# Performance work log

Measured on AMD Instinct MI355X. Metric: run time of the kernel, lower is better.

The kernel has to match this reference:

```python
import jax, jax.numpy as jnp
import numpy as np

# Mamba2 derived dims (headdim=64, ngroups=1, mamba_ssm defaults)
D_MODEL = 1024
D_STATE = 64
D_CONV = 4
EXPAND = 2
D_INNER = EXPAND * D_MODEL          # 2048
HEADDIM = 64
NHEADS = D_INNER // HEADDIM          # 32
CONV_DIM = D_INNER + 2 * D_STATE     # 2176 (x, B, C share the depthwise conv)
D_IN_PROJ = 2 * D_INNER + 2 * D_STATE + NHEADS  # 4256 (z, xBC, dt)
BATCH, SEQ = 8, 1024


def setup_inputs() -> dict:
    key = jax.random.key(0)
    ks = jax.random.split(key, 8)
    g = lambda k, shp, sc=0.02: (jax.random.normal(k, shp, jnp.float32) * sc)
    # dt_bias init as in mamba_ssm: inverse-softplus of dt ~ U[1e-3, 1e-1] (log-uniform)
    dt = jnp.exp(jax.random.uniform(ks[3], (NHEADS,), jnp.float32)
                 * (jnp.log(0.1) - jnp.log(0.001)) + jnp.log(0.001))
    dt_bias = dt + jnp.log(-jnp.expm1(-dt))  # softplus^{-1}(dt)
    A_log = jnp.log(jax.random.uniform(ks[4], (NHEADS,), jnp.float32, 1.0, 16.0))
    return {
        "x": jax.random.normal(ks[0], (BATCH, SEQ, D_MODEL), jnp.float32),
        "W_in": g(ks[1], (D_MODEL, D_IN_PROJ)),
        "conv_w": g(ks[2], (D_CONV, CONV_DIM), 0.2),
        "conv_b": jnp.zeros((CONV_DIM,), jnp.float32),
        "dt_bias": dt_bias,
        "A_log": A_log,
        "Dskip": jnp.ones((NHEADS,), jnp.float32),
        "norm_w": jnp.ones((D_INNER,), jnp.float32),
        "W_out": g(ks[5], (D_INNER, D_MODEL)),
        "head_w": g(ks[6], (D_MODEL, 1)),
        "head_b": jnp.zeros((1,), jnp.float32),
    }


def _mamba2(x, W_in, conv_w, conv_b, dt_bias, A_log, Dskip, norm_w, W_out):
    b, l, _ = x.shape
    zxbcdt = x @ W_in                                   # (b, l, 4256)
    z = zxbcdt[..., :D_INNER]
    xBC = zxbcdt[..., D_INNER:D_INNER + CONV_DIM]
    dt = jax.nn.softplus(zxbcdt[..., D_INNER + CONV_DIM:] + dt_bias)  # (b, l, h)
    # causal depthwise conv1d (kernel D_CONV) + SiLU
    pad = jnp.pad(xBC, ((0, 0), (D_CONV - 1, 0), (0, 0)))
    conv = conv_b + sum(pad[:, k:k + l, :] * conv_w[k] for k in range(D_CONV))
    xBC = jax.nn.silu(conv)
    xh = xBC[..., :D_INNER].reshape(b, l, NHEADS, HEADDIM)
    B = xBC[..., D_INNER:D_INNER + D_STATE]             # (b, l, s) ngroups=1
    C = xBC[..., D_INNER + D_STATE:]                    # (b, l, s)
    A = -jnp.exp(A_log)                                 # (h,)
    dA = jnp.exp(dt * A)                                # (b, l, h)

    def step(h, inps):
        dA_t, dt_t, B_t, C_t, x_t = inps                # (b,h),(b,h),(b,s),(b,s),(b,h,p)
        h = h * dA_t[:, :, None, None] + (dt_t[:, :, None] * x_t)[..., None] * B_t[:, None, None, :]
        y = jnp.einsum('bhps,bs->bhp', h, C_t)
        return h, y

    tm = lambda a: jnp.moveaxis(a, 1, 0)                # time-major for scan
    h0 = jnp.zeros((b, NHEADS, HEADDIM, D_STATE), x.dtype)
    _, y = jax.lax.scan(step, h0, (tm(dA), tm(dt), tm(B), tm(C), tm(xh)))
    y = jnp.moveaxis(y, 0, 1) + Dskip[None, None, :, None] * xh   # skip connection
    # gated RMSNorm: norm(y * silu(z)) * weight
    y = y.reshape(b, l, D_INNER) * jax.nn.silu(z)
    y = y * jax.lax.rsqrt(jnp.mean(y * y, axis=-1, keepdims=True) + 1e-5) * norm_w
    return y @ W_out                                    # (b, l, d_model)


def reference(x, W_in, conv_w, conv_b, dt_bias, A_log, Dskip, norm_w, W_out, head_w, head_b):
    y = _mamba2(x, W_in, conv_w, conv_b, dt_bias, A_log, Dskip, norm_w, W_out)
    return y @ head_w + head_b                          # (b, l, 1)
```

## Files before the change

### kernel.cpp

```cpp
#include <hip/hip_runtime.h>
#include <hip/hip_bf16.h>

#define D_MODEL   1024
#define D_STATE   64
#define D_INNER   2048
#define NHEADS    32
#define CONV_DIM  2176
#define D_IN_PROJ 4256
#define NPAD      4352
#define BATCH     8
#define SEQ       1024
#define NROWS     8192
#define NCHUNK    8
#define CLEN      128

typedef __attribute__((ext_vector_type(8))) short bf16x8;
typedef __attribute__((ext_vector_type(4))) float f32x4;

__device__ __forceinline__ float bf2f(unsigned short u){
  unsigned v = ((unsigned)u) << 16;
  return __builtin_bit_cast(float, v);
}
__device__ __forceinline__ unsigned short f2bf(float f){
  __hip_bfloat16 h = __float2bfloat16(f);
  return __builtin_bit_cast(unsigned short, h);
}

__global__ __launch_bounds__(256) void k_convert_x(const float* __restrict__ x,
                                                   unsigned short* __restrict__ xb){
  int i = blockIdx.x*256 + threadIdx.x;
  float4 v = ((const float4*)x)[i];
  ushort4 o;
  o.x = f2bf(v.x); o.y = f2bf(v.y); o.z = f2bf(v.z); o.w = f2bf(v.w);
  ((ushort4*)xb)[i] = o;
}

__global__ __launch_bounds__(256) void k_transpose_win(const float* __restrict__ W_in,
                                                       unsigned short* __restrict__ wt){
  __shared__ float tile[32][33];
  int n0 = blockIdx.x * 32;
  int k0 = blockIdx.y * 32;
  int tx = threadIdx.x & 31;
  int ty = threadIdx.x >> 5;
  #pragma unroll
  for (int i = 0; i < 4; ++i){
    int kk = ty + i*8;
    int n  = n0 + tx;
    tile[kk][tx] = (n < D_IN_PROJ) ? W_in[(size_t)(k0+kk)*D_IN_PROJ + n] : 0.f;
  }
  __syncthreads();
  #pragma unroll
  for (int i = 0; i < 4; ++i){
    int nn = ty + i*8;
    wt[(size_t)(n0+nn)*D_MODEL + k0 + tx] = f2bf(tile[tx][nn]);
  }
}

__global__ __launch_bounds__(256) void k_nwc(const float* __restrict__ W_out,
                                             const float* __restrict__ head_w,
                                             const float* __restrict__ norm_w,
                                             float* __restrict__ nwc){
  int d    = blockIdx.x*4 + (threadIdx.x >> 6);
  int lane = threadIdx.x & 63;
  const float* row = W_out + (size_t)d * D_MODEL;
  float s = 0.f;
  #pragma unroll
  for (int k = lane; k < D_MODEL; k += 64) s += row[k] * head_w[k];
  #pragma unroll
  for (int off = 32; off; off >>= 1) s += __shfl_down(s, off);
  if (lane == 0) nwc[d] = s * norm_w[d];
}

__global__ __launch_bounds__(256) void k_gemm_bf16_bt(const unsigned short* __restrict__ A,
                                                      const unsigned short* __restrict__ BT,
                                                      unsigned short* __restrict__ C,
                                                      int M, int N, int K){
  __shared__ unsigned short aT[128*64];
  __shared__ unsigned short bT[128*64];
  int nb   = N >> 7;
  int bid  = blockIdx.x;
  int swz  = (bid & 7) * (gridDim.x >> 3) + (bid >> 3);
  int m0   = (swz / nb) << 7;
  int n0   = (swz % nb) << 7;
  int tid  = threadIdx.x;
  int wid  = tid >> 6, lane = tid & 63;
  int wr   = wid >> 1, wc = wid & 1;

  f32x4 acc[4][4];
  #pragma unroll
  for (int i = 0; i < 4; ++i)
    #pragma unroll
    for (int j = 0; j < 4; ++j)
      acc[i][j] = (f32x4){0.f, 0.f, 0.f, 0.f};

  int frow = lane & 15;
  int fk   = (lane >> 4) << 3;
  int srow = lane >> 3;
  int skk  = (lane & 7) << 3;

  for (int k0 = 0; k0 < K; k0 += 64){
    __syncthreads();
    #pragma unroll
    for (int it = 0; it < 4; ++it){
      int ch  = (wid << 2) | it;
      int row = (ch << 3) | srow;
      __builtin_amdgcn_global_load_lds(
        (const __attribute__((address_space(1))) void*)(A  + (size_t)(m0+row)*K + k0 + skk),
        (__attribute__((address_space(3))) void*)(aT + (ch << 9)), 16, 0, 0);
      __builtin_amdgcn_global_load_lds(
        (const __attribute__((address_space(1))) void*)(BT + (size_t)(n0+row)*K + k0 + skk),
        (__attribute__((address_space(3))) void*)(bT + (ch << 9)), 16, 0, 0);
    }
    __syncthreads();
    #pragma unroll
    for (int kk = 0; kk < 64; kk += 32){
      bf16x8 af[4], bfv[4];
      #pragma unroll
      for (int i = 0; i < 4; ++i)
        af[i]  = *(const bf16x8*)(aT + ((wr*64 + i*16 + frow) << 6) + kk + fk);
      #pragma unroll
      for (int j = 0; j < 4; ++j)
        bfv[j] = *(const bf16x8*)(bT + ((wc*64 + j*16 + frow) << 6) + kk + fk);
      #pragma unroll
      for (int i = 0; i < 4; ++i)
        #pragma unroll
        for (int j = 0; j < 4; ++j)
          acc[i][j] = __builtin_amdgcn_mfma_f32_16x16x32_bf16(af[i], bfv[j], acc[i][j], 0, 0, 0);
    }
  }

  int crow = (lane >> 4) << 2;
  int ccol = lane & 15;
  #pragma unroll
  for (int i = 0; i < 4; ++i)
    #pragma unroll
    for (int j = 0; j < 4; ++j){
      size_t base = (size_t)(m0 + wr*64 + i*16 + crow) * N + (n0 + wc*64 + j*16 + ccol);
      #pragma unroll
      for (int r = 0; r < 4; ++r)
        C[base + (size_t)r * N] = f2bf(acc[i][j][r]);
    }
}

__global__ __launch_bounds__(256) void k_dtda(const unsigned short* __restrict__ zx,
                                              const float* __restrict__ dt_bias,
                                              float* __restrict__ dtb){
  int i = blockIdx.x*256 + threadIdx.x;
  int r = i >> 5, h = i & 31;
  float raw = bf2f(zx[(size_t)r*NPAD + D_INNER + CONV_DIM + h]) + dt_bias[h];
  float dt  = (raw > 20.f) ? raw : log1pf(expf(raw));
  int b = r >> 10, l = r & 1023;
  dtb[(b*32 + h)*1024 + l] = dt;
}

__global__ __launch_bounds__(256) void k_conv(const unsigned short* __restrict__ zx,
                                              const float* __restrict__ conv_w,
                                              const float* __restrict__ conv_b,
                                              unsigned short* __restrict__ xbc,
                                              unsigned short* __restrict__ bc16){
  int r = blockIdx.x;
  int l = r & (SEQ - 1);
  for (int oc = threadIdx.x; oc < 272; oc += 256){
    int c = oc * 8;
    float acc[8];
    #pragma unroll
    for (int j = 0; j < 8; ++j) acc[j] = conv_b[c + j];
    #pragma unroll
    for (int k = 0; k < 4; ++k){
      int dl = l + k - 3;
      if (dl >= 0){
        bf16x8 v = *(const bf16x8*)(zx + (size_t)(r + k - 3)*NPAD + D_INNER + c);
        #pragma unroll
        for (int j = 0; j < 8; ++j)
          acc[j] = fmaf(bf2f((unsigned short)v[j]), conv_w[k*CONV_DIM + c + j], acc[j]);
      }
    }
    bf16x8 o;
    #pragma unroll
    for (int j = 0; j < 8; ++j){
      float s = acc[j] / (1.f + expf(-acc[j]));
      o[j] = (short)f2bf(s);
    }
    if (c < D_INNER) *(bf16x8*)(xbc  + (size_t)r*D_INNER + c) = o;
    else             *(bf16x8*)(bc16 + (size_t)r*128 + (c - D_INNER)) = o;
  }
}

__global__ __launch_bounds__(64) void k_cs(const float* __restrict__ dtb,
                                           const float* __restrict__ A_log,
                                           float* __restrict__ csb,
                                           float* __restrict__ cumA){
  int id = blockIdx.x;
  int bh = id >> 3, c = id & 7;
  int h  = bh & 31;
  int l  = threadIdx.x;
  const float* src = dtb + (size_t)bh*1024 + (c << 7);
  float d0 = src[2*l], d1 = src[2*l + 1];
  float pr = d0 + d1;
  float s  = pr;
  #pragma unroll
  for (int off = 1; off < 64; off <<= 1){
    float n = __shfl_up(s, off);
    if (l >= off) s += n;
  }
  float excl = s - pr;
  csb[(size_t)id*128 + 2*l]     = excl + d0;
  csb[(size_t)id*128 + 2*l + 1] = excl + pr;
  if (l == 63){
    float A = -expf(A_log[h]);
    cumA[id] = expf(A * s);
  }
}

__global__ __launch_bounds__(256) void k_ssd1(const unsigned short* __restrict__ xbc,
                                              const unsigned short* __restrict__ bc16,
                                              const float* __restrict__ dtb,
                                              const float* __restrict__ csb,
                                              const float* __restrict__ A_log,
                                              unsigned short* __restrict__ hend){
  __shared__ __align__(16) unsigned short XTw[64*136];
  __shared__ __align__(16) unsigned short BTl[64*136];
  int id = blockIdx.x;
  int bh = id >> 3, c = id & 7;
  int b  = bh >> 5, h = bh & 31;
  int tid = threadIdx.x;
  int w = tid >> 6, l = tid & 63;
  float A = -expf(A_log[h]);
  int row0 = b*SEQ + (c << 7);
  float csT = csb[(size_t)id*128 + 127];

  #pragma unroll
  for (int it = 0; it < 4; ++it){
    int idx = it*256 + tid;
    int tau = idx >> 3, pb = idx & 7;
    bf16x8 v = *(const bf16x8*)(xbc + (size_t)(row0+tau)*D_INNER + h*64 + pb*8);
    float wgt = dtb[(size_t)bh*1024 + (c<<7) + tau]
              * expf(A*(csT - csb[(size_t)id*128 + tau]));
    #pragma unroll
    for (int j = 0; j < 8; ++j)
      XTw[(pb*8+j)*136 + tau] = f2bf(bf2f((unsigned short)v[j]) * wgt);
  }
  #pragma unroll
  for (int it = 0; it < 4; ++it){
    int idx = it*256 + tid;
    int tau = idx >> 3, sb = idx & 7;
    bf16x8 v = *(const bf16x8*)(bc16 + (size_t)(row0+tau)*128 + sb*8);
    #pragma unroll
    for (int j = 0; j < 8; ++j)
      BTl[(sb*8+j)*136 + tau] = (unsigned short)v[j];
  }
  __syncthreads();

  int fr = l & 15, fo = (l >> 4) << 3;
  f32x4 acc[4];
  #pragma unroll
  for (int n = 0; n < 4; ++n) acc[n] = (f32x4){0.f,0.f,0.f,0.f};
  #pragma unroll
  for (int kt = 0; kt < 4; ++kt){
    bf16x8 pf = *(const bf16x8*)(XTw + (w*16+fr)*136 + kt*32 + fo);
    #pragma unroll
    for (int n = 0; n < 4; ++n){
      bf16x8 qf = *(const bf16x8*)(BTl + (n*16+fr)*136 + kt*32 + fo);
      acc[n] = __builtin_amdgcn_mfma_f32_16x16x32_bf16(pf, qf, acc[n], 0, 0, 0);
    }
  }
  #pragma unroll
  for (int n = 0; n < 4; ++n)
    #pragma unroll
    for (int r = 0; r < 4; ++r){
      int p = w*16 + ((l>>4)<<2) + r;
      int s = n*16 + fr;
      hend[(size_t)id*4096 + p*64 + s] = f2bf(acc[n][r]);
    }
}

__global__ __launch_bounds__(256) void k_comb(unsigned short* __restrict__ hh,
                                              const float* __restrict__ cumA){
  int bh = blockIdx.x, tid = threadIdx.x;
  float carry[16];
  #pragma unroll
  for (int i = 0; i < 16; ++i) carry[i] = 0.f;
  #pragma unroll
  for (int c = 0; c < NCHUNK; ++c){
    size_t base = (((size_t)bh*NCHUNK + c) << 12) + tid*16;
    bf16x8 a0 = *(const bf16x8*)(hh + base);
    bf16x8 a1 = *(const bf16x8*)(hh + base + 8);
    float ca = cumA[bh*NCHUNK + c];
    float tmp[16];
    #pragma unroll
    for (int i = 0; i < 8; ++i){
      tmp[i]   = bf2f((unsigned short)a0[i]);
      tmp[8+i] = bf2f((unsigned short)a1[i]);
    }
    bf16x8 w0, w1;
    #pragma unroll
    for (int i = 0; i < 8; ++i){
      w0[i] = (short)f2bf(carry[i]);
      w1[i] = (short)f2bf(carry[8+i]);
    }
    *(bf16x8*)(hh + base)     = w0;
    *(bf16x8*)(hh + base + 8) = w1;
    #pragma unroll
    for (int i = 0; i < 16; ++i) carry[i] = tmp[i] + ca*carry[i];
  }
}

__global__ __launch_bounds__(256) void k_ssd2(const unsigned short* __restrict__ xbc,
                                              const unsigned short* __restrict__ bc16,
                                              const float* __restrict__ dtb,
                                              const float* __restrict__ csb,
                                              const float* __restrict__ A_log,
                                              const float* __restrict__ Dskip,
                                              const unsigned short* __restrict__ hbuf,
                                              unsigned short* __restrict__ yb){
  __shared__ __align__(16) unsigned short Bl[128*72];
  __shared__ __align__(16) unsigned short Cl[128*72];
  __shared__ __align__(16) unsigned short XTl[64*136];
  __shared__ __align__(16) unsigned short hl[64*72];
  __shared__ __align__(16) unsigned short Gm[128*136];
  __shared__ float cs_l[128], dt_l[128], a_l[128];

  int id = blockIdx.x;
  int bh = id >> 3, c = id & 7;
  int b  = bh >> 5, h = bh & 31;
  int tid = threadIdx.x;
  int w = tid >> 6, l = tid & 63;
  float A = -expf(A_log[h]);
  int row0 = b*SEQ + (c << 7);

  #pragma unroll
  for (int it = 0; it < 8; ++it){
    int idx = it*256 + tid;
    int tau = idx >> 4, cb = idx & 15;
    bf16x8 v = *(const bf16x8*)(bc16 + (size_t)(row0+tau)*128 + cb*8);
    unsigned short* dst = (cb < 8) ? (Bl + tau*72 + cb*8)
                                   : (Cl + tau*72 + (cb-8)*8);
    *(bf16x8*)dst = v;
  }
  #pragma unroll
  for (int it = 0; it < 4; ++it){
    int idx = it*256 + tid;
    int tau = idx >> 3, pb = idx & 7;
    bf16x8 v = *(const bf16x8*)(xbc + (size_t)(row0+tau)*D_INNER + h*64 + pb*8);
    #pragma unroll
    for (int j = 0; j < 8; ++j)
      XTl[(pb*8+j)*136 + tau] = (unsigned short)v[j];
  }
  #pragma unroll
  for (int it = 0; it < 2; ++it){
    int idx = it*256 + tid;
    int p = idx >> 3, sb = idx & 7;
    bf16x8 v = *(const bf16x8*)(hbuf + (size_t)id*4096 + p*64 + sb*8);
    *(bf16x8*)(hl + p*72 + sb*8) = v;
  }
  if (tid < 128){
    float cs = csb[(size_t)id*128 + tid];
    cs_l[tid] = cs;
    dt_l[tid] = dtb[(size_t)bh*1024 + (c<<7) + tid];
    a_l[tid]  = expf(A*cs);
  }
  __syncthreads();

  int fr = l & 15, fo = (l >> 4) << 3;
  int mtB = 7 - w;

  f32x4 Y[2][4];
  #pragma unroll
  for (int mi = 0; mi < 2; ++mi)
    #pragma unroll
    for (int n = 0; n < 4; ++n) Y[mi][n] = (f32x4){0.f,0.f,0.f,0.f};
  #pragma unroll
  for (int mi = 0; mi < 2; ++mi){
    int mt = mi ? mtB : w;
    #pragma unroll
    for (int kt = 0; kt < 2; ++kt){
      bf16x8 pf = *(const bf16x8*)(Cl + (mt*16+fr)*72 + kt*32 + fo);
      #pragma unroll
      for (int n = 0; n < 4; ++n){
        bf16x8 qf = *(const bf16x8*)(hl + (n*16+fr)*72 + kt*32 + fo);
        Y[mi][n] = __builtin_amdgcn_mfma_f32_16x16x32_bf16(pf, qf, Y[mi][n], 0, 0, 0);
      }
    }
    #pragma unroll
    for (int r = 0; r < 4; ++r){
      float av = a_l[mt*16 + ((l>>4)<<2) + r];
      #pragma unroll
      for (int n = 0; n < 4; ++n) Y[mi][n][r] *= av;
    }
  }

  f32x4 Sv[9];
  #pragma unroll
  for (int slot = 0; slot < 9; ++slot){
    int mt = (slot <= w) ? w : mtB;
    int nt = (slot <= w) ? slot : slot - w - 1;
    f32x4 acc = (f32x4){0.f,0.f,0.f,0.f};
    #pragma unroll
    for (int kt = 0; kt < 2; ++kt){
      bf16x8 pf = *(const bf16x8*)(Cl + (mt*16+fr)*72 + kt*32 + fo);
      bf16x8 qf = *(const bf16x8*)(Bl + (nt*16+fr)*72 + kt*32 + fo);
      acc = __builtin_amdgcn_mfma_f32_16x16x32_bf16(pf, qf, acc, 0, 0, 0);
    }
    int tau = nt*16 + fr;
    float dtt = dt_l[tau];
    float cst = cs_l[tau];
    #pragma unroll
    for (int r = 0; r < 4; ++r){
      int t = mt*16 + ((l>>4)<<2) + r;
      float v = acc[r] * dtt * expf(A*(cs_l[t] - cst));
      acc[r] = (tau <= t) ? v : 0.f;
    }
    Sv[slot] = acc;
  }

  __syncthreads();

  #pragma unroll
  for (int slot = 0; slot < 9; ++slot){
    int mt = (slot <= w) ? w : mtB;
    int nt = (slot <= w) ? slot : slot - w - 1;
    int tau = nt*16 + fr;
    #pragma unroll
    for (int r = 0; r < 4; ++r){
      int t = mt*16 + ((l>>4)<<2) + r;
      Gm[t*136 + tau] = f2bf(Sv[slot][r]);
    }
  }
  {
    int mtE = (w & 1) ? mtB : w;
    int ntE = mtE + 1;
    #pragma unroll
    for (int r = 0; r < 4; ++r){
      int t = mtE*16 + ((l>>4)<<2) + r;
      Gm[t*136 + ntE*16 + fr] = 0;
    }
  }
  __syncthreads();

  #pragma unroll
  for (int mi = 0; mi < 2; ++mi){
    int mt = mi ? mtB : w;
    int kmax = (mt + 2) >> 1;
    for (int kt2 = 0; kt2 < kmax; ++kt2){
      bf16x8 pf = *(const bf16x8*)(Gm + (mt*16+fr)*136 + kt2*32 + fo);
      #pragma unroll
      for (int n = 0; n < 4; ++n){
        bf16x8 qf = *(const bf16x8*)(XTl + (n*16+fr)*136 + kt2*32 + fo);
        Y[mi][n] = __builtin_amdgcn_mfma_f32_16x16x32_bf16(pf, qf, Y[mi][n], 0, 0, 0);
      }
    }
  }

  float dsk = Dskip[h];
  #pragma unroll
  for (int mi = 0; mi < 2; ++mi){
    int mt = mi ? mtB : w;
    #pragma unroll
    for (int r = 0; r < 4; ++r){
      int t = mt*16 + ((l>>4)<<2) + r;
      size_t orow = (size_t)(row0 + t)*D_INNER + h*64;
      #pragma unroll
      for (int n = 0; n < 4; ++n){
        int p = n*16 + fr;
        float xv = bf2f(XTl[p*136 + t]);
        yb[orow + p] = f2bf(Y[mi][n][r] + dsk*xv);
      }
    }
  }
}

__global__ __launch_bounds__(256) void k_epilogue(const unsigned short* __restrict__ y,
                                                  const unsigned short* __restrict__ zx,
                                                  const float* __restrict__ nwc,
                                                  const float* __restrict__ head_b,
                                                  float* __restrict__ out){
  int r   = blockIdx.x;
  int tid = threadIdx.x;
  bf16x8 y8 = *(const bf16x8*)(y  + (size_t)r*D_INNER + tid*8);
  bf16x8 z8 = *(const bf16x8*)(zx + (size_t)r*NPAD   + tid*8);
  float4 w0 = ((const float4*)nwc)[tid*2];
  float4 w1 = ((const float4*)nwc)[tid*2 + 1];
  float wv[8] = {w0.x, w0.y, w0.z, w0.w, w1.x, w1.y, w1.z, w1.w};
  float s2 = 0.f, sd = 0.f;
  #pragma unroll
  for (int k = 0; k < 8; ++k){
    float yf = bf2f((unsigned short)y8[k]);
    float zf = bf2f((unsigned short)z8[k]);
    float g  = yf * (zf / (1.f + expf(-zf)));
    s2 += g*g; sd += g*wv[k];
  }
  #pragma unroll
  for (int off = 32; off; off >>= 1){
    s2 += __shfl_down(s2, off);
    sd += __shfl_down(sd, off);
  }
  __shared__ float r2[4], rd[4];
  if ((tid & 63) == 0){ r2[tid >> 6] = s2; rd[tid >> 6] = sd; }
  __syncthreads();
  if (tid == 0){
    float t2 = r2[0] + r2[1] + r2[2] + r2[3];
    float td = rd[0] + rd[1] + rd[2] + rd[3];
    out[r] = rsqrtf(t2 * (1.f/2048.f) + 1e-5f) * td + head_b[0];
  }
}

extern "C" void kernel_launch(void* const* d_in, const int* in_sizes, int n_in,
                              void* d_out, int out_size, void* d_ws, size_t ws_size,
                              hipStream_t stream){
  const float* x       = (const float*)d_in[0];
  const float* W_in    = (const float*)d_in[1];
  const float* conv_w  = (const float*)d_in[2];
  const float* conv_b  = (const float*)d_in[3];
  const float* dt_bias = (const float*)d_in[4];
  const float* A_log   = (const float*)d_in[5];
  const float* Dskip   = (const float*)d_in[6];
  const float* norm_w  = (const float*)d_in[7];
  const float* W_out   = (const float*)d_in[8];
  const float* head_w  = (const float*)d_in[9];
  const float* head_b  = (const float*)d_in[10];
  float* out = (float*)d_out;

  char* ws = (char*)d_ws;
  unsigned short* xb   = (unsigned short*)(ws + 0);
  unsigned short* wt   = (unsigned short*)(ws + 16777216);
  unsigned short* zx16 = (unsigned short*)(ws + 25690112);
  unsigned short* xbc  = (unsigned short*)(ws + 96993280);
  float*          dtb  = (float*)         (ws + 132644864);
  float*          nwc  = (float*)         (ws + 134742016);
  unsigned short* yb   = (unsigned short*)(ws + 134750208);

  unsigned short* hbuf = xb;
  unsigned short* bc16 = wt;
  float*          csb  = (float*)(ws + 16777216 + 2097152);
  float*          cumA = (float*)(ws + 16777216 + 3145728);

  k_convert_x<<<8192, 256, 0, stream>>>(x, xb);
  k_transpose_win<<<dim3(136, 32), 256, 0, stream>>>(W_in, wt);
  k_nwc<<<512, 256, 0, stream>>>(W_out, head_w, norm_w, nwc);
  k_gemm_bf16_bt<<<(NROWS/128)*(NPAD/128), 256, 0, stream>>>(xb, wt, zx16, NROWS, NPAD, D_MODEL);
  k_dtda<<<1024, 256, 0, stream>>>(zx16, dt_bias, dtb);
  k_conv<<<NROWS, 256, 0, stream>>>(zx16, conv_w, conv_b, xbc, bc16);
  k_cs<<<2048, 64, 0, stream>>>(dtb, A_log, csb, cumA);
  k_ssd1<<<2048, 256, 0, stream>>>(xbc, bc16, dtb, csb, A_log, hbuf);
  k_comb<<<256, 256, 0, stream>>>(hbuf, cumA);
  k_ssd2<<<2048, 256, 0, stream>>>(xbc, bc16, dtb, csb, A_log, Dskip, hbuf, yb);
  k_epilogue<<<NROWS, 256, 0, stream>>>(yb, zx16, nwc, head_b, out);
}
```

Before: 280.4 us.

## Replace input-projection GEMM with 256x256 double-buffered tile kernel

Result: no change. 284.4 us (+1.4%).

```diff
diff --git a/kernel.cpp b/kernel.cpp
--- a/kernel.cpp
+++ b/kernel.cpp
@@ -71,74 +71,88 @@
   if (lane == 0) nwc[d] = s * norm_w[d];
 }
 
-__global__ __launch_bounds__(256) void k_gemm_bf16_bt(const unsigned short* __restrict__ A,
-                                                      const unsigned short* __restrict__ BT,
-                                                      unsigned short* __restrict__ C,
-                                                      int M, int N, int K){
-  __shared__ unsigned short aT[128*64];
-  __shared__ unsigned short bT[128*64];
-  int nb   = N >> 7;
+__global__ __launch_bounds__(512, 1) void k_gemm256(const unsigned short* __restrict__ A,
+                                                    const unsigned short* __restrict__ BT,
+                                                    unsigned short* __restrict__ C){
+  __shared__ unsigned short smem[65536];
   int bid  = blockIdx.x;
-  int swz  = (bid & 7) * (gridDim.x >> 3) + (bid >> 3);
-  int m0   = (swz / nb) << 7;
-  int n0   = (swz % nb) << 7;
+  int m0   = (bid / 17) << 8;
+  int n0   = (bid % 17) << 8;
   int tid  = threadIdx.x;
-  int wid  = tid >> 6, lane = tid & 63;
-  int wr   = wid >> 1, wc = wid & 1;
-
-  f32x4 acc[4][4];
-  #pragma unroll
-  for (int i = 0; i < 4; ++i)
-    #pragma unroll
-    for (int j = 0; j < 4; ++j)
-      acc[i][j] = (f32x4){0.f, 0.f, 0.f, 0.f};
-
-  int frow = lane & 15;
-  int fk   = (lane >> 4) << 3;
-  int srow = lane >> 3;
-  int skk  = (lane & 7) << 3;
-
-  for (int k0 = 0; k0 < K; k0 += 64){
-    __syncthreads();
-    #pragma unroll
-    for (int it = 0; it < 4; ++it){
-      int ch  = (wid << 2) | it;
-      int row = (ch << 3) | srow;
-      __builtin_amdgcn_global_load_lds(
-        (const __attribute__((address_space(1))) void*)(A  + (size_t)(m0+row)*K + k0 + skk),
-        (__attribute__((address_space(3))) void*)(aT + (ch << 9)), 16, 0, 0);
-      __builtin_amdgcn_global_load_lds(
-        (const __attribute__((address_space(1))) void*)(BT + (size_t)(n0+row)*K + k0 + skk),
-        (__attribute__((address_space(3))) void*)(bT + (ch << 9)), 16, 0, 0);
-    }
-    __syncthreads();
+  int w    = tid >> 6, lane = tid & 63;
+  int wr   = w >> 2, wc = w & 3;
+  int stR  = tid >> 3;
+  int stC  = (tid & 7) << 3;
+  int wb   = w << 9;
+
+  f32x4 acc[8][4];
+  #pragma unroll
+  for (int i = 0; i < 8; ++i)
+    #pragma unroll
+    for (int j = 0; j < 4; ++j) acc[i][j] = (f32x4){0.f,0.f,0.f,0.f};
+
+  const unsigned short* sA0 = A  + (size_t)(m0 + stR)*D_MODEL + stC;
+  const unsigned short* sB0 = BT + (size_t)(n0 + stR)*D_MODEL + stC;
+
+#define STAGE256(bb, kt) { \
+    const unsigned short* pa = sA0 + (size_t)(kt)*64; \
+    const unsigned short* pb = sB0 + (size_t)(kt)*64; \
+    _Pragma("unroll") \
+    for (int it = 0; it < 4; ++it){ \
+      __builtin_amdgcn_global_load_lds((const __attribute__((address_space(1))) void*)(pa + (size_t)it*64*D_MODEL), \
+          (__attribute__((address_space(3))) void*)(smem + (bb)*32768 + it*4096 + wb), 16, 0, 0); \
+      __builtin_amdgcn_global_load_lds((const __attribute__((address_space(1))) void*)(pb + (size_t)it*64*D_MODEL), \
+          (__attribute__((address_space(3))) void*)(smem + (bb)*32768 + 16384 + it*4096 + wb), 16, 0, 0); \
+    } }
+
+  STAGE256(0, 0);
+
+  int frow = lane & 15, fk = (lane >> 4) << 3;
+
+  for (int t = 0; t < 16; ++t){
+    int cur = t & 1;
+    asm volatile("" ::: "memory");
+    __builtin_amdgcn_s_barrier();
+    if (t < 15){
+      STAGE256(cur ^ 1, t + 1);
+      asm volatile("s_waitcnt vmcnt(8)" ::: "memory");
+    } else {
+      asm volatile("s_waitcnt vmcnt(0)" ::: "memory");
+    }
+    __builtin_amdgcn_s_barrier();
+    asm volatile("" ::: "memory");
+
+    const unsigned short* At = smem + cur*32768;
+    const unsigned short* Bt = At + 16384;
+    __builtin_amdgcn_s_setprio(1);
     #pragma unroll
     for (int kk = 0; kk < 64; kk += 32){
-      bf16x8 af[4], bfv[4];
-      #pragma unroll
-      for (int i = 0; i < 4; ++i)
-        af[i]  = *(const bf16x8*)(aT + ((wr*64 + i*16 + frow) << 6) + kk + fk);
-      #pragma unroll
-      for (int j = 0; j < 4; ++j)
-        bfv[j] = *(const bf16x8*)(bT + ((wc*64 + j*16 + frow) << 6) + kk + fk);
-      #pragma unroll
-      for (int i = 0; i < 4; ++i)
+      bf16x8 af[8], bfr[4];
+      #pragma unroll
+      for (int mf = 0; mf < 8; ++mf)
+        af[mf] = *(const bf16x8*)(At + (wr*128 + mf*16 + frow)*64 + kk + fk);
+      #pragma unroll
+      for (int nf = 0; nf < 4; ++nf)
+        bfr[nf] = *(const bf16x8*)(Bt + (wc*64 + nf*16 + frow)*64 + kk + fk);
+      #pragma unroll
+      for (int mf = 0; mf < 8; ++mf)
         #pragma unroll
-        for (int j = 0; j < 4; ++j)
-          acc[i][j] = __builtin_amdgcn_mfma_f32_16x16x32_bf16(af[i], bfv[j], acc[i][j], 0, 0, 0);
-    }
-  }
-
-  int crow = (lane >> 4) << 2;
-  int ccol = lane & 15;
-  #pragma unroll
-  for (int i = 0; i < 4; ++i)
-    #pragma unroll
-    for (int j = 0; j < 4; ++j){
-      size_t base = (size_t)(m0 + wr*64 + i*16 + crow) * N + (n0 + wc*64 + j*16 + ccol);
+        for (int nf = 0; nf < 4; ++nf)
+          acc[mf][nf] = __builtin_amdgcn_mfma_f32_16x16x32_bf16(af[mf], bfr[nf], acc[mf][nf], 0, 0, 0);
+    }
+    __builtin_amdgcn_s_setprio(0);
+  }
+#undef STAGE256
+
+  int crow = (lane >> 4) << 2, ccol = lane & 15;
+  #pragma unroll
+  for (int mf = 0; mf < 8; ++mf)
+    #pragma unroll
+    for (int nf = 0; nf < 4; ++nf){
+      size_t base = (size_t)(m0 + wr*128 + mf*16 + crow)*NPAD + (n0 + wc*64 + nf*16 + ccol);
       #pragma unroll
       for (int r = 0; r < 4; ++r)
-        C[base + (size_t)r * N] = f2bf(acc[i][j][r]);
+        C[base + (size_t)r*NPAD] = f2bf(acc[mf][nf][r]);
     }
 }
 
@@ -537,7 +551,7 @@
   k_convert_x<<<8192, 256, 0, stream>>>(x, xb);
   k_transpose_win<<<dim3(136, 32), 256, 0, stream>>>(W_in, wt);
   k_nwc<<<512, 256, 0, stream>>>(W_out, head_w, norm_w, nwc);
-  k_gemm_bf16_bt<<<(NROWS/128)*(NPAD/128), 256, 0, stream>>>(xb, wt, zx16, NROWS, NPAD, D_MODEL);
+  k_gemm256<<<(NROWS/256)*(NPAD/256), 512, 0, stream>>>(xb, wt, zx16);
   k_dtda<<<1024, 256, 0, stream>>>(zx16, dt_bias, dtb);
   k_conv<<<NROWS, 256, 0, stream>>>(zx16, conv_w, conv_b, xbc, bc16);
   k_cs<<<2048, 64, 0, stream>>>(dtb, A_log, csb, cumA);
```
